# Optimization experiments

Hardware: AMD Instinct MI355X
Metric: run time of the kernel (lower is better)

## Reference

```python
import jax, jax.numpy as jnp
import numpy as np

D_MODEL = 2048
N_HEADS = 16
N_KV_HEADS = 4
HEAD_DIM = D_MODEL // N_HEADS  # 128
ROPE_BASE = 10000.0


def _rope_tables(T, head_dim):
    half = head_dim // 2
    theta = 1.0 / (ROPE_BASE ** (jnp.arange(half, dtype=jnp.float32) / half))
    m = jnp.arange(T, dtype=jnp.float32)
    freqs = jnp.outer(m, theta)  # (T, half)
    return jnp.cos(freqs), jnp.sin(freqs)


def _apply_rope(x, cos, sin):
    # x: (B, H, T, hd); rotate first/second halves as pairs
    half = x.shape[-1] // 2
    x1, x2 = x[..., :half], x[..., half:]
    cos = cos[None, None, :, :]
    sin = sin[None, None, :, :]
    return jnp.concatenate([x1 * cos - x2 * sin, x1 * sin + x2 * cos], axis=-1)


def setup_inputs() -> dict:
    key = jax.random.key(0)
    ks = jax.random.split(key, 5)
    B, T = 4, 2048
    x = jax.random.normal(ks[0], (B, T, D_MODEL), dtype=jnp.float32)
    Wq = jax.random.normal(ks[1], (D_MODEL, N_HEADS * HEAD_DIM), dtype=jnp.float32) * 0.02
    Wk = jax.random.normal(ks[2], (D_MODEL, N_KV_HEADS * HEAD_DIM), dtype=jnp.float32) * 0.02
    Wv = jax.random.normal(ks[3], (D_MODEL, N_KV_HEADS * HEAD_DIM), dtype=jnp.float32) * 0.02
    Wo = jax.random.normal(ks[4], (N_HEADS * HEAD_DIM, D_MODEL), dtype=jnp.float32) * (0.02 / np.sqrt(2.0))
    return {"x": x, "Wq": Wq, "Wk": Wk, "Wv": Wv, "Wo": Wo}


def reference(x, Wq, Wk, Wv, Wo):
    B, T, C = x.shape
    groups = N_HEADS // N_KV_HEADS

    # QKV projections
    q = (x @ Wq).reshape(B, T, N_HEADS, HEAD_DIM).transpose(0, 2, 1, 3)      # (B,H,T,hd)
    k = (x @ Wk).reshape(B, T, N_KV_HEADS, HEAD_DIM).transpose(0, 2, 1, 3)   # (B,Hkv,T,hd)
    v = (x @ Wv).reshape(B, T, N_KV_HEADS, HEAD_DIM).transpose(0, 2, 1, 3)

    # RoPE on q and k
    cos, sin = _rope_tables(T, HEAD_DIM)
    q = _apply_rope(q, cos, sin)
    k = _apply_rope(k, cos, sin)

    # GQA: repeat each kv head `groups` times
    k = jnp.repeat(k, groups, axis=1)  # (B,H,T,hd)
    v = jnp.repeat(v, groups, axis=1)

    # Attention scores with ALiBi bias and causal mask
    scale = 1.0 / np.sqrt(HEAD_DIM)
    scores = jnp.einsum('bhqd,bhkd->bhqk', q, k) * scale  # (B,H,T,T)

    pos = jnp.arange(T)
    dist = jnp.minimum(pos[None, :] - pos[:, None], 0).astype(jnp.float32)  # (T,T), <=0
    slopes = 2.0 ** (-8.0 * jnp.arange(1, N_HEADS + 1, dtype=jnp.float32) / N_HEADS)
    alibi = slopes[:, None, None] * dist[None, :, :]  # (H,T,T)
    scores = scores + alibi[None]

    causal = pos[None, :] > pos[:, None]  # True = future = blocked
    scores = jnp.where(causal[None, None], -jnp.inf, scores)

    weights = jax.nn.softmax(scores, axis=-1)
    out = jnp.einsum('bhqk,bhkd->bhqd', weights, v)  # (B,H,T,hd)
    out = out.transpose(0, 2, 1, 3).reshape(B, T, N_HEADS * HEAD_DIM)
    return out @ Wo
```

## Files before the change

kernel.cpp:

```cpp
#include <hip/hip_runtime.h>
#include <hip/hip_bf16.h>
#include <stdint.h>

#define T_SEQ 2048
#define DM    2048
#define NH    16
#define NKVH  4
#define HD    128
#define NBATCH 4
#define BT    (NBATCH * T_SEQ)
#define ATT_SCALE 0.08838834764831845f
#define LOG2E 1.4426950408889634f

typedef __attribute__((ext_vector_type(8))) short bf16x8;
typedef __attribute__((ext_vector_type(4))) float f32x4;
typedef __attribute__((ext_vector_type(16))) float f32x16;
typedef __attribute__((ext_vector_type(8))) unsigned short ushort8;
typedef __attribute__((ext_vector_type(4))) unsigned short ushort4v;

static __device__ __forceinline__ unsigned short f2bf(float f) {
  __hip_bfloat16 h = __float2bfloat16(f);
  return __builtin_bit_cast(unsigned short, h);
}
static __device__ __forceinline__ float bf2f(unsigned short u) {
  unsigned int v = ((unsigned int)u) << 16;
  return __builtin_bit_cast(float, v);
}
static __device__ __forceinline__ unsigned int cvtpk(float a, float b) {
  unsigned int r;
  asm("v_cvt_pk_bf16_f32 %0, %1, %2" : "=v"(r) : "v"(a), "v"(b));
  return r;
}

#define GLDS16(g, l)                                                        \
  __builtin_amdgcn_global_load_lds(                                         \
      (const __attribute__((address_space(1))) void*)(g),                   \
      (__attribute__((address_space(3))) void*)(l), 16, 0, 0)

__global__ __launch_bounds__(256) void castx_k(const float* __restrict__ x,
                                               unsigned short* __restrict__ xb) {
  int i = (blockIdx.x * 256 + threadIdx.x) * 4;
  float4 v = *(const float4*)&x[i];
  ushort4v o;
  o[0] = f2bf(v.x); o[1] = f2bf(v.y); o[2] = f2bf(v.z); o[3] = f2bf(v.w);
  *(ushort4v*)&xb[i] = o;
}

__global__ __launch_bounds__(256) void transw_k(const float* __restrict__ src,
                                                unsigned short* __restrict__ dst,
                                                int ncols) {
  __shared__ unsigned short t[64][72];
  int n0 = blockIdx.x * 64, r0 = blockIdx.y * 64;
  int tid = threadIdx.x;
  int tx = tid & 15, ty = tid >> 4;
#pragma unroll
  for (int i = 0; i < 4; i++) {
    int r = ty * 4 + i;
    float4 v = *(const float4*)&src[(size_t)(r0 + r) * ncols + n0 + tx * 4];
    t[r][tx * 4 + 0] = f2bf(v.x);
    t[r][tx * 4 + 1] = f2bf(v.y);
    t[r][tx * 4 + 2] = f2bf(v.z);
    t[r][tx * 4 + 3] = f2bf(v.w);
  }
  __syncthreads();
  int nl = tid >> 2, seg = tid & 3;
  ushort8 o0, o1;
#pragma unroll
  for (int j = 0; j < 8; j++) {
    o0[j] = t[seg * 16 + j][nl];
    o1[j] = t[seg * 16 + 8 + j][nl];
  }
  size_t base = (size_t)(n0 + nl) * 2048 + r0 + seg * 16;
  *(ushort8*)&dst[base] = o0;
  *(ushort8*)&dst[base + 8] = o1;
}

template <int EPI, int NBY, int BYG>
__global__ __launch_bounds__(512) void gemm8_k(const unsigned short* __restrict__ A,
                                               const unsigned short* __restrict__ Bt,
                                               unsigned short* __restrict__ q_out,
                                               unsigned short* __restrict__ k_out,
                                               unsigned short* __restrict__ v_out,
                                               float* __restrict__ f_out) {
  __shared__ __align__(16) unsigned short smem[65536];

  const int tid = threadIdx.x;
  const int lane = tid & 63, wid = tid >> 6;
  const int wm = wid >> 2, wn = wid & 3;
  const int lr = lane & 15, lq = lane >> 4;
  const int sw = ((lr >> 2) & 1) << 1;

  const int k8 = blockIdx.x & 7;
  const int l = blockIdx.x >> 3;
  const int gi = l / (4 * BYG);
  const int t4 = l % (4 * BYG);
  const int bx = k8 * 4 + (t4 & 3);
  const int by = gi * BYG + (t4 >> 2);
  const int row0 = bx * 256, n00 = by * 256;

  const int clog = (tid & 7) ^ (((tid >> 5) & 1) << 1);
  const unsigned short* Asrc = A + (size_t)row0 * 2048 + clog * 8;
  const unsigned short* Bsrc = Bt + (size_t)n00 * 2048 + clog * 8;

  auto stageA = [&](int buf, int h, int k0) {
#pragma unroll
    for (int c = 0; c < 2; c++) {
      const int rl = c * 128 + h * 64 + (tid >> 3);
      GLDS16(Asrc + (size_t)rl * 2048 + k0,
             &smem[buf * 32768 + (c * 128 + h * 64) * 64 + tid * 8]);
    }
  };
  auto stageB = [&](int buf, int h, int k0) {
#pragma unroll
    for (int c = 0; c < 2; c++) {
      const int pr = h * 128 + c * 64 + (tid >> 3);
      const int p = pr >> 5;
      const int lg = (p < 4) ? (2 * p) : (2 * (p - 4) + 1);
      const int logical = lg * 32 + (pr & 31);
      GLDS16(Bsrc + (size_t)logical * 2048 + k0,
             &smem[buf * 32768 + 16384 + (h * 128 + c * 64) * 64 + tid * 8]);
    }
  };

  auto ldA = [&](int buf, int rl, int kh) -> bf16x8 {
    return *(const bf16x8*)&smem[buf * 32768 + rl * 64 + (((kh << 2) + lq) ^ sw) * 8];
  };
  auto ldB = [&](int buf, int ni, int kh) -> bf16x8 {
    const int p = (ni < 2) ? wn : (4 + wn);
    const int pr = p * 32 + (ni & 1) * 16 + lr;
    return *(const bf16x8*)&smem[buf * 32768 + 16384 + pr * 64 +
                                 (((kh << 2) + lq) ^ sw) * 8];
  };

  f32x4 acc[8][4] = {};

  stageA(0, 0, 0);
  stageB(0, 0, 0);
  stageB(0, 1, 0);
  stageA(0, 1, 0);

  bf16x8 af[4][2], bfr[4][2];

#pragma unroll 1
  for (int t = 0; t < 32; ++t) {
    const int buf = t & 1, obuf = buf ^ 1;
    const bool nx = (t + 1 < 32);
    const int k0n = (t + 1) << 6;

    asm volatile("s_waitcnt vmcnt(4)" ::: "memory");
    asm volatile("s_barrier" ::: "memory");
#pragma unroll
    for (int m = 0; m < 4; m++)
#pragma unroll
      for (int kh = 0; kh < 2; kh++) af[m][kh] = ldA(buf, wm * 128 + m * 16 + lr, kh);
#pragma unroll
    for (int ni = 0; ni < 2; ni++)
#pragma unroll
      for (int kh = 0; kh < 2; kh++) bfr[ni][kh] = ldB(buf, ni, kh);
    if (nx) stageA(obuf, 0, k0n);
    __builtin_amdgcn_s_setprio(1);
#pragma unroll
    for (int m = 0; m < 4; m++)
#pragma unroll
      for (int ni = 0; ni < 2; ni++)
#pragma unroll
        for (int kh = 0; kh < 2; kh++)
          acc[m][ni] = __builtin_amdgcn_mfma_f32_16x16x32_bf16(af[m][kh], bfr[ni][kh],
                                                               acc[m][ni], 0, 0, 0);
    __builtin_amdgcn_s_setprio(0);

    if (nx) asm volatile("s_waitcnt vmcnt(4)" ::: "memory");
    else    asm volatile("s_waitcnt vmcnt(2)" ::: "memory");
    asm volatile("s_barrier" ::: "memory");
#pragma unroll
    for (int ni = 2; ni < 4; ni++)
#pragma unroll
      for (int kh = 0; kh < 2; kh++) bfr[ni][kh] = ldB(buf, ni, kh);
    if (nx) stageB(obuf, 0, k0n);
    __builtin_amdgcn_s_setprio(1);
#pragma unroll
    for (int m = 0; m < 4; m++)
#pragma unroll
      for (int ni = 2; ni < 4; ni++)
#pragma unroll
        for (int kh = 0; kh < 2; kh++)
          acc[m][ni] = __builtin_amdgcn_mfma_f32_16x16x32_bf16(af[m][kh], bfr[ni][kh],
                                                               acc[m][ni], 0, 0, 0);
    __builtin_amdgcn_s_setprio(0);

    if (nx) asm volatile("s_waitcnt vmcnt(4)" ::: "memory");
    else    asm volatile("s_waitcnt vmcnt(0)" ::: "memory");
    asm volatile("s_barrier" ::: "memory");
#pragma unroll
    for (int m = 0; m < 4; m++)
#pragma unroll
      for (int kh = 0; kh < 2; kh++)
        af[m][kh] = ldA(buf, wm * 128 + 64 + m * 16 + lr, kh);
    if (nx) stageB(obuf, 1, k0n);
    __builtin_amdgcn_s_setprio(1);
#pragma unroll
    for (int m = 0; m < 4; m++)
#pragma unroll
      for (int ni = 0; ni < 2; ni++)
#pragma unroll
        for (int kh = 0; kh < 2; kh++)
          acc[4 + m][ni] = __builtin_amdgcn_mfma_f32_16x16x32_bf16(
              af[m][kh], bfr[ni][kh], acc[4 + m][ni], 0, 0, 0);
    __builtin_amdgcn_s_setprio(0);

    asm volatile("s_barrier" ::: "memory");
    if (nx) stageA(obuf, 1, k0n);
    __builtin_amdgcn_s_setprio(1);
#pragma unroll
    for (int m = 0; m < 4; m++)
#pragma unroll
      for (int ni = 2; ni < 4; ni++)
#pragma unroll
        for (int kh = 0; kh < 2; kh++)
          acc[4 + m][ni] = __builtin_amdgcn_mfma_f32_16x16x32_bf16(
              af[m][kh], bfr[ni][kh], acc[4 + m][ni], 0, 0, 0);
    __builtin_amdgcn_s_setprio(0);
  }

  const int rbase = row0 + wm * 128;
  const int cbase = n00 + wn * 64;
#pragma unroll
  for (int mi = 0; mi < 8; mi++)
#pragma unroll
    for (int ni = 0; ni < 4; ni++)
#pragma unroll
      for (int r = 0; r < 4; r++) {
        int row = rbase + mi * 16 + lq * 4 + r;
        int col = cbase + ni * 16 + lr;
        float v = acc[mi][ni][r];
        if (EPI == 0) {
          if (col < 2048) {
            q_out[(size_t)row * 2048 + col] = f2bf(v);
          } else if (col < 2560) {
            k_out[(size_t)row * 512 + (col - 2048)] = f2bf(v);
          } else {
            int nv = col - 2560;
            int kvh = nv >> 7, d = nv & 127;
            int b = row >> 11, tt = row & 2047;
            v_out[((size_t)(b * NKVH + kvh) * HD + d) * T_SEQ + tt] = f2bf(v);
          }
        } else {
          f_out[(size_t)row * 2048 + col] = v;
        }
      }
}

__global__ __launch_bounds__(256) void rope_tab_k(float2* __restrict__ tab) {
  int idx = blockIdx.x * 256 + threadIdx.x;
  int t = idx >> 6, i = idx & 63;
  float theta = exp2f(-(float)i * (13.287712379549449f / 64.0f));
  float s, c;
  sincosf((float)t * theta, &s, &c);
  tab[idx] = make_float2(c, s);
}

__global__ __launch_bounds__(256) void rope_k(unsigned short* __restrict__ qb,
                                              unsigned short* __restrict__ kb,
                                              const float2* __restrict__ tab) {
  int idx = blockIdx.x * 256 + threadIdx.x;
  int i = idx & 63;
  int wi = idx >> 6;
  int hh = wi % (NH + NKVH);
  int bt = wi / (NH + NKVH);
  int t = bt & (T_SEQ - 1);
  unsigned short* p = (hh < NH) ? (qb + (size_t)bt * 2048 + hh * HD)
                                : (kb + (size_t)bt * 512 + (hh - NH) * HD);
  float2 cs = tab[(t << 6) + i];
  float x1 = bf2f(p[i]), x2 = bf2f(p[i + 64]);
  p[i] = f2bf(x1 * cs.x - x2 * cs.y);
  p[i + 64] = f2bf(x1 * cs.y + x2 * cs.x);
}

__global__ __launch_bounds__(256) void attn_k(const unsigned short* __restrict__ qb,
                                              const unsigned short* __restrict__ kb,
                                              const unsigned short* __restrict__ vt,
                                              unsigned short* __restrict__ ao) {
  __shared__ __align__(16) unsigned short smem[24576];

  const int bid = blockIdx.x;
  const int j = 15 - (bid >> 6);
  const int g = (bid & 7) | (((bid >> 3) & 1) << 3);
  const int hh = (bid >> 4) & 3;
  const int b = g >> 2, kvh = g & 3;
  const int h = kvh * 4 + hh;

  const int tid = threadIdx.x;
  const int wid = tid >> 6, lane = tid & 63;
  const int l31 = lane & 31, lh = lane >> 5;
  const int xr = l31 & 7;
  const float slope2 = exp2f(-0.5f * (float)(h + 1)) * LOG2E;
  const float scale2 = ATT_SCALE * LOG2E;

  const int q0 = j * 128 + wid * 32;
  const int dt_w = j * 4 + wid;
  const int nt = j * 4 + 4;

  const int krow = tid >> 4;
  const int cgk = (tid & 15) ^ (krow & 7);
  const int vr = tid >> 3;
  const int cgv = (tid & 7) ^ (vr & 7);

  const unsigned short* khead = kb + (size_t)(b * T_SEQ) * 512 + kvh * 128;
  const unsigned short* vhead = vt + (size_t)(b * NKVH + kvh) * HD * T_SEQ;

  auto stage = [&](int slot, int tile) {
    const int k0 = tile * 32;
    unsigned short* base = &smem[slot * 8192];
    GLDS16(khead + (size_t)(k0 + krow) * 512 + cgk * 8, base + tid * 8);
    GLDS16(khead + (size_t)(k0 + 16 + krow) * 512 + cgk * 8, base + 2048 + tid * 8);
    GLDS16(vhead + (size_t)(((cgv >> 2) << 6) + vr) * T_SEQ + k0 + (cgv & 3) * 8,
           base + 4096 + tid * 8);
    GLDS16(vhead + (size_t)(((cgv >> 2) << 6) + 32 + vr) * T_SEQ + k0 + (cgv & 3) * 8,
           base + 6144 + tid * 8);
  };

  unsigned short (*ot)[32][136] = (unsigned short(*)[32][136])smem;

  const unsigned short* qrow =
      qb + ((size_t)(b * T_SEQ + q0 + l31)) * 2048 + h * HD + lh * 8;
  bf16x8 qf[8];
#pragma unroll
  for (int ds = 0; ds < 8; ds++) qf[ds] = *(const bf16x8*)&qrow[ds * 16];

  f32x16 oacc[4] = {};
  float m2 = -1e30f, l_half = 0.f;
  const float arow = -slope2 * (float)(q0 + l31);

  float cr[16];
#pragma unroll
  for (int r = 0; r < 16; r++) {
    const int crow = (r & 3) + 8 * (r >> 2) + 4 * lh;
    cr[r] = fmaf(slope2, (float)crow, arow);
  }

  stage(0, nt - 1);
  stage(1, nt - 2);

#pragma unroll 1
  for (int it = 0; it < nt; ++it) {
    const int tt = nt - 1 - it;
    if (it == nt - 1) {
      asm volatile("s_waitcnt vmcnt(0)" ::: "memory");
    } else {
      asm volatile("s_waitcnt vmcnt(4)" ::: "memory");
    }
    asm volatile("s_barrier" ::: "memory");
    if (tt >= 2) stage((it + 2) % 3, tt - 2);

    if (tt <= dt_w) {
      const int slot = it % 3;
      const unsigned short* Kb = &smem[slot * 8192];
      const unsigned short* Vb = &smem[slot * 8192 + 4096];
      const int k0 = tt * 32;

      bf16x8 kf[8];
#pragma unroll
      for (int ds = 0; ds < 8; ds++)
        kf[ds] = *(const bf16x8*)&Kb[l31 * 128 + ((2 * ds + lh) ^ xr) * 8];

      __builtin_amdgcn_s_setprio(1);
      f32x16 sca = 0.f, scb = 0.f;
#pragma unroll
      for (int ds = 0; ds < 4; ds++)
        sca = __builtin_amdgcn_mfma_f32_32x32x16_bf16(kf[ds], qf[ds], sca, 0, 0, 0);
#pragma unroll
      for (int ds = 4; ds < 8; ds++)
        scb = __builtin_amdgcn_mfma_f32_32x32x16_bf16(kf[ds], qf[ds], scb, 0, 0, 0);
      __builtin_amdgcn_s_setprio(0);

      bf16x8 vf[4][2];
#pragma unroll
      for (int dt = 0; dt < 4; dt++)
#pragma unroll
        for (int ks = 0; ks < 2; ks++)
          vf[dt][ks] = *(const bf16x8*)&Vb[((dt & 1) * 32 + l31) * 64 +
                                           (((dt >> 1) * 4 + 2 * ks + lh) ^ xr) * 8];

      float s1[16];
#pragma unroll
      for (int r = 0; r < 16; r++) s1[r] = fmaf(sca[r] + scb[r], scale2, cr[r]);
      if (tt == dt_w) {
#pragma unroll
        for (int r = 0; r < 16; r++) {
          const int crow = (r & 3) + 8 * (r >> 2) + 4 * lh;
          if (crow > l31) s1[r] = -1e30f;
        }
      }

      float z = fmaf(slope2, (float)k0, -m2);

      float t8[8], t4[4];
#pragma unroll
      for (int i = 0; i < 8; i++) t8[i] = fmaxf(s1[i], s1[i + 8]);
#pragma unroll
      for (int i = 0; i < 4; i++) t4[i] = fmaxf(t8[i], t8[i + 4]);
      float mx = fmaxf(fmaxf(t4[0], t4[1]), fmaxf(t4[2], t4[3]));

      float pr[16];
#pragma unroll
      for (int r = 0; r < 16; r++) pr[r] = exp2f(s1[r] + z);

      mx = fmaxf(mx, __shfl_xor(mx, 32));
      if (__any(mx + z > 8.f)) {
        const float mt = (mx + z) + m2;
        const float mnew = fmaxf(m2, mt);
        const float corr = exp2f(m2 - mnew);
        l_half *= corr;
#pragma unroll
        for (int dt = 0; dt < 4; dt++) oacc[dt] *= corr;
        m2 = mnew;
        z = fmaf(slope2, (float)k0, -m2);
#pragma unroll
        for (int r = 0; r < 16; r++) pr[r] = exp2f(s1[r] + z);
      }

      float a8[8], a4[4];
#pragma unroll
      for (int i = 0; i < 8; i++) a8[i] = pr[i] + pr[i + 8];
#pragma unroll
      for (int i = 0; i < 4; i++) a4[i] = a8[i] + a8[i + 4];
      l_half += (a4[0] + a4[1]) + (a4[2] + a4[3]);

      unsigned int w[8];
#pragma unroll
      for (int i = 0; i < 8; i++) w[i] = cvtpk(pr[2 * i], pr[2 * i + 1]);
      const unsigned int ta = __shfl_xor(lh ? w[0] : w[2], 32);
      const unsigned int tb = __shfl_xor(lh ? w[1] : w[3], 32);
      const unsigned int tc = __shfl_xor(lh ? w[4] : w[6], 32);
      const unsigned int td = __shfl_xor(lh ? w[5] : w[7], 32);
      union U4 { unsigned int u[4]; bf16x8 v; } f0, f1;
      f0.u[0] = lh ? ta : w[0];
      f0.u[1] = lh ? tb : w[1];
      f0.u[2] = lh ? w[2] : ta;
      f0.u[3] = lh ? w[3] : tb;
      f1.u[0] = lh ? tc : w[4];
      f1.u[1] = lh ? td : w[5];
      f1.u[2] = lh ? w[6] : tc;
      f1.u[3] = lh ? w[7] : td;

      __builtin_amdgcn_s_setprio(1);
#pragma unroll
      for (int dt = 0; dt < 4; dt++) {
        oacc[dt] =
            __builtin_amdgcn_mfma_f32_32x32x16_bf16(vf[dt][0], f0.v, oacc[dt], 0, 0, 0);
        oacc[dt] =
            __builtin_amdgcn_mfma_f32_32x32x16_bf16(vf[dt][1], f1.v, oacc[dt], 0, 0, 0);
      }
      __builtin_amdgcn_s_setprio(0);
    }
  }

  const float l_tot = l_half + __shfl_xor(l_half, 32);
  const float inv = 1.0f / l_tot;
  __syncthreads();
#pragma unroll
  for (int dt = 0; dt < 4; dt++)
#pragma unroll
    for (int rg = 0; rg < 4; rg++) {
      ushort4v o;
#pragma unroll
      for (int jj = 0; jj < 4; jj++) o[jj] = f2bf(oacc[dt][rg * 4 + jj] * inv);
      *(ushort4v*)&ot[wid][l31][dt * 32 + rg * 8 + lh * 4] = o;
    }
  __syncthreads();
  const int rrow = lane >> 4, chunk = lane & 15;
#pragma unroll
  for (int ps = 0; ps < 8; ps++) {
    const int row = ps * 4 + rrow;
    ushort8 v = *(const ushort8*)&ot[wid][row][chunk * 8];
    *(ushort8*)&ao[((size_t)(b * T_SEQ + q0 + row)) * 2048 + h * HD + chunk * 8] = v;
  }
}

extern "C" void kernel_launch(void* const* d_in, const int* in_sizes, int n_in,
                              void* d_out, int out_size, void* d_ws, size_t ws_size,
                              hipStream_t stream) {
  const float* x = (const float*)d_in[0];
  const float* Wq = (const float*)d_in[1];
  const float* Wk = (const float*)d_in[2];
  const float* Wv = (const float*)d_in[3];
  const float* Wo = (const float*)d_in[4];

  char* w = (char*)d_ws;
  unsigned short* xb = (unsigned short*)w;
  unsigned short* wqt = (unsigned short*)(w + 33554432);
  unsigned short* qb = (unsigned short*)(w + 33554432 + 12582912);
  unsigned short* kb = (unsigned short*)(w + 33554432 + 12582912 + 33554432);
  unsigned short* vtb = (unsigned short*)(w + 33554432 + 12582912 + 33554432 + 8388608);
  float2* rtab = (float2*)w;

  castx_k<<<16384, 256, 0, stream>>>(x, xb);
  transw_k<<<dim3(32, 32), 256, 0, stream>>>(Wq, wqt, 2048);
  transw_k<<<dim3(8, 32), 256, 0, stream>>>(Wk, wqt + (size_t)2048 * 2048, 512);
  transw_k<<<dim3(8, 32), 256, 0, stream>>>(Wv, wqt + (size_t)2560 * 2048, 512);
  gemm8_k<0, 12, 3><<<384, 512, 0, stream>>>(xb, wqt, qb, kb, vtb, nullptr);
  rope_tab_k<<<512, 256, 0, stream>>>(rtab);
  rope_k<<<40960, 256, 0, stream>>>(qb, kb, rtab);
  transw_k<<<dim3(32, 32), 256, 0, stream>>>(Wo, wqt, 2048);
  attn_k<<<1024, 256, 0, stream>>>(qb, kb, vtb, xb);
  gemm8_k<1, 8, 4><<<256, 512, 0, stream>>>(xb, wqt, nullptr, nullptr, nullptr,
                                            (float*)d_out);
}
```

Before: 450.6 us.

## Fuse Q RoPE into attention prologue and merge QKV weight transposes

Applies RoPE to the query fragment in registers inside the attention kernel, reading cos/sin from the table, so the standalone rope pass only rotates K. This removes a full read-modify-write pass over Q in global memory. The three Wq/Wk/Wv transpose launches are merged into one, and the K/V staging loads are issued before the Q load so they overlap the rotation. The rope table moves to a workspace offset that no longer aliases xb, because attention now reads it while xb holds the attention output. Attention blocks recompute the Q rotation redundantly, adding table loads and registers to the prologue.

```diff
diff --git a/kernel.cpp b/kernel.cpp
--- a/kernel.cpp
+++ b/kernel.cpp
@@ -44,6 +44,47 @@
   ushort4v o;
   o[0] = f2bf(v.x); o[1] = f2bf(v.y); o[2] = f2bf(v.z); o[3] = f2bf(v.w);
   *(ushort4v*)&xb[i] = o;
+}
+
+__global__ __launch_bounds__(256) void transqkv_k(const float* __restrict__ Wq,
+                                                  const float* __restrict__ Wk,
+                                                  const float* __restrict__ Wv,
+                                                  unsigned short* __restrict__ wqt) {
+  __shared__ unsigned short t[64][72];
+  const int bx = blockIdx.x;
+  const float* src;
+  unsigned short* dst;
+  int ncols, n0;
+  if (bx < 32) {
+    src = Wq; dst = wqt; ncols = 2048; n0 = bx * 64;
+  } else if (bx < 40) {
+    src = Wk; dst = wqt + (size_t)2048 * 2048; ncols = 512; n0 = (bx - 32) * 64;
+  } else {
+    src = Wv; dst = wqt + (size_t)2560 * 2048; ncols = 512; n0 = (bx - 40) * 64;
+  }
+  const int r0 = blockIdx.y * 64;
+  const int tid = threadIdx.x;
+  const int tx = tid & 15, ty = tid >> 4;
+#pragma unroll
+  for (int i = 0; i < 4; i++) {
+    int r = ty * 4 + i;
+    float4 v = *(const float4*)&src[(size_t)(r0 + r) * ncols + n0 + tx * 4];
+    t[r][tx * 4 + 0] = f2bf(v.x);
+    t[r][tx * 4 + 1] = f2bf(v.y);
+    t[r][tx * 4 + 2] = f2bf(v.z);
+    t[r][tx * 4 + 3] = f2bf(v.w);
+  }
+  __syncthreads();
+  int nl = tid >> 2, seg = tid & 3;
+  ushort8 o0, o1;
+#pragma unroll
+  for (int j = 0; j < 8; j++) {
+    o0[j] = t[seg * 16 + j][nl];
+    o1[j] = t[seg * 16 + 8 + j][nl];
+  }
+  size_t base = (size_t)(n0 + nl) * 2048 + r0 + seg * 16;
+  *(ushort8*)&dst[base] = o0;
+  *(ushort8*)&dst[base + 8] = o1;
 }
 
 __global__ __launch_bounds__(256) void transw_k(const float* __restrict__ src,
@@ -259,17 +300,15 @@
   tab[idx] = make_float2(c, s);
 }
 
-__global__ __launch_bounds__(256) void rope_k(unsigned short* __restrict__ qb,
-                                              unsigned short* __restrict__ kb,
-                                              const float2* __restrict__ tab) {
+__global__ __launch_bounds__(256) void ropek_k(unsigned short* __restrict__ kb,
+                                               const float2* __restrict__ tab) {
   int idx = blockIdx.x * 256 + threadIdx.x;
   int i = idx & 63;
   int wi = idx >> 6;
-  int hh = wi % (NH + NKVH);
-  int bt = wi / (NH + NKVH);
+  int kvh = wi & 3;
+  int bt = wi >> 2;
   int t = bt & (T_SEQ - 1);
-  unsigned short* p = (hh < NH) ? (qb + (size_t)bt * 2048 + hh * HD)
-                                : (kb + (size_t)bt * 512 + (hh - NH) * HD);
+  unsigned short* p = kb + (size_t)bt * 512 + kvh * HD;
   float2 cs = tab[(t << 6) + i];
   float x1 = bf2f(p[i]), x2 = bf2f(p[i + 64]);
   p[i] = f2bf(x1 * cs.x - x2 * cs.y);
@@ -279,6 +318,7 @@
 __global__ __launch_bounds__(256) void attn_k(const unsigned short* __restrict__ qb,
                                               const unsigned short* __restrict__ kb,
                                               const unsigned short* __restrict__ vt,
+                                              const float2* __restrict__ rtab,
                                               unsigned short* __restrict__ ao) {
   __shared__ __align__(16) unsigned short smem[24576];
 
@@ -321,12 +361,29 @@
 
   unsigned short (*ot)[32][136] = (unsigned short(*)[32][136])smem;
 
+  stage(0, nt - 1);
+  stage(1, nt - 2);
+
   const unsigned short* qrow =
       qb + ((size_t)(b * T_SEQ + q0 + l31)) * 2048 + h * HD + lh * 8;
   bf16x8 qf[8];
 #pragma unroll
   for (int ds = 0; ds < 8; ds++) qf[ds] = *(const bf16x8*)&qrow[ds * 16];
 
+  {
+    const float2* rt = rtab + ((q0 + l31) << 6) + lh * 8;
+#pragma unroll
+    for (int ds = 0; ds < 4; ds++)
+#pragma unroll
+      for (int e = 0; e < 8; e++) {
+        float2 cs = rt[ds * 16 + e];
+        float x1 = bf2f((unsigned short)qf[ds][e]);
+        float x2 = bf2f((unsigned short)qf[ds + 4][e]);
+        qf[ds][e] = (short)f2bf(x1 * cs.x - x2 * cs.y);
+        qf[ds + 4][e] = (short)f2bf(x1 * cs.y + x2 * cs.x);
+      }
+  }
+
   f32x16 oacc[4] = {};
   float m2 = -1e30f, l_half = 0.f;
   const float arow = -slope2 * (float)(q0 + l31);
@@ -337,9 +394,6 @@
     const int crow = (r & 3) + 8 * (r >> 2) + 4 * lh;
     cr[r] = fmaf(slope2, (float)crow, arow);
   }
-
-  stage(0, nt - 1);
-  stage(1, nt - 2);
 
 #pragma unroll 1
   for (int it = 0; it < nt; ++it) {
@@ -492,17 +546,15 @@
   unsigned short* qb = (unsigned short*)(w + 33554432 + 12582912);
   unsigned short* kb = (unsigned short*)(w + 33554432 + 12582912 + 33554432);
   unsigned short* vtb = (unsigned short*)(w + 33554432 + 12582912 + 33554432 + 8388608);
-  float2* rtab = (float2*)w;
+  float2* rtab = (float2*)(w + 33554432 + 8388608);
 
   castx_k<<<16384, 256, 0, stream>>>(x, xb);
-  transw_k<<<dim3(32, 32), 256, 0, stream>>>(Wq, wqt, 2048);
-  transw_k<<<dim3(8, 32), 256, 0, stream>>>(Wk, wqt + (size_t)2048 * 2048, 512);
-  transw_k<<<dim3(8, 32), 256, 0, stream>>>(Wv, wqt + (size_t)2560 * 2048, 512);
+  transqkv_k<<<dim3(48, 32), 256, 0, stream>>>(Wq, Wk, Wv, wqt);
   gemm8_k<0, 12, 3><<<384, 512, 0, stream>>>(xb, wqt, qb, kb, vtb, nullptr);
   rope_tab_k<<<512, 256, 0, stream>>>(rtab);
-  rope_k<<<40960, 256, 0, stream>>>(qb, kb, rtab);
+  ropek_k<<<8192, 256, 0, stream>>>(kb, rtab);
   transw_k<<<dim3(32, 32), 256, 0, stream>>>(Wo, wqt, 2048);
-  attn_k<<<1024, 256, 0, stream>>>(qb, kb, vtb, xb);
+  attn_k<<<1024, 256, 0, stream>>>(qb, kb, vtb, rtab, xb);
   gemm8_k<1, 8, 4><<<256, 512, 0, stream>>>(xb, wqt, nullptr, nullptr, nullptr,
                                             (float*)d_out);
 }
```

Result: no change. 442.2 us, median of 2 (-1.9%).
